# Performance work log

Hardware: AMD Instinct MI355X
Metric: run time of the kernel (lower is better)

## Reference

```python
import jax, jax.numpy as jnp
import numpy as np

N_NODES = 128
F = 64            # hidden channels (64x0e + 64x1o)
N_RBF = 8
H_R = 64          # radial MLP hidden
L = 2             # num_interactions
R_MAX = 5.0
AVG_NEIGH = 127.0
G_DIM = 16
N_SPECIES = 5

# static fully-connected edge list (no self edges): E = n*(n-1)
_idx = np.arange(N_NODES)
_s, _r = np.meshgrid(_idx, _idx, indexing='ij')
_mask = _s != _r
SENDERS = jnp.asarray(_s[_mask])    # [E]
RECEIVERS = jnp.asarray(_r[_mask])  # [E]


def setup_inputs() -> dict:
    key = jax.random.key(0)
    ks = jax.random.split(key, 12)
    inp = {
        'positions': jax.random.normal(ks[0], (32, N_NODES, 3), jnp.float32),
        'node_features': jax.random.randint(ks[1], (32, N_NODES), 0, N_SPECIES),
        'global_features': jax.random.normal(ks[2], (32, G_DIM), jnp.float32),
        # learned parameters
        'embed': jax.random.normal(ks[3], (N_SPECIES, F), jnp.float32) * 0.1,
        'glob_w': jax.random.normal(ks[4], (G_DIM, F), jnp.float32) * 0.1,
        'rbf_w1': jax.random.normal(ks[5], (L, N_RBF, H_R), jnp.float32) * 0.3,
        'rbf_b1': jnp.zeros((L, H_R), jnp.float32),
        'rbf_w2': jax.random.normal(ks[6], (L, H_R, 3 * F), jnp.float32) * 0.1,
        'ws': jax.random.normal(ks[7], (L, F, F), jnp.float32) * 0.1,
        'wv': jax.random.normal(ks[8], (L, F, F), jnp.float32) * 0.1,
        'wout': jax.random.normal(ks[9], (F,), jnp.float32) * 0.1,
        'final_scaling': jnp.ones((), jnp.float32),
    }
    return inp


def _rbf(d):
    # gaussian radial basis on [0, r_max]
    centers = jnp.linspace(0.0, R_MAX, N_RBF)
    width = R_MAX / N_RBF
    return jnp.exp(-((d[:, None] - centers) ** 2) / (2.0 * width * width))  # [E, N_RBF]


def _single(pos, species, glob, embed, glob_w, rbf_w1, rbf_b1, rbf_w2, ws, wv, wout, final_scaling):
    # graph construction + edge vectors
    edge_vec = pos[RECEIVERS] - pos[SENDERS]                 # [E,3]
    d = jnp.sqrt(jnp.sum(edge_vec ** 2, axis=-1) + 1e-12)   # [E]
    unit = edge_vec / d[:, None]                             # [E,3]
    phi = _rbf(d)                                            # [E,N_RBF]

    # node embedding (species one-hot lookup) conditioned on global features
    s = embed[species] + glob @ glob_w                       # [n,F] scalars
    v = jnp.zeros((N_NODES, F, 3), pos.dtype)                # [n,F,3] vectors

    for l in range(L):
        rw = jax.nn.silu(phi @ rbf_w1[l] + rbf_b1[l]) @ rbf_w2[l]  # [E,3F]
        r1, r2, r3 = jnp.split(rw, 3, axis=-1)               # each [E,F]
        ms = r1 * s[SENDERS]                                 # [E,F]
        mv = r2[..., None] * v[SENDERS] + (r3 * s[SENDERS])[..., None] * unit[:, None, :]  # [E,F,3]
        agg_s = jax.ops.segment_sum(ms, RECEIVERS, num_segments=N_NODES) / AVG_NEIGH
        agg_v = jax.ops.segment_sum(mv, RECEIVERS, num_segments=N_NODES) / AVG_NEIGH
        s = s + agg_s @ ws[l]
        v = v + jnp.einsum('nfd,fg->ngd', agg_v, wv[l])

    out = jnp.einsum('nfd,f->nd', v, wout)                   # equivariant readout [n,3]
    return (out - pos) * final_scaling


def reference(positions, node_features, global_features, embed, glob_w, rbf_w1,
              rbf_b1, rbf_w2, ws, wv, wout, final_scaling):
    fn = lambda p, sp, g: _single(p, sp, g, embed, glob_w, rbf_w1, rbf_b1,
                                  rbf_w2, ws, wv, wout, final_scaling)
    return jax.vmap(fn)(positions, node_features, global_features)
```

## Files before the change

kernel.cpp:

```cpp
#include <hip/hip_runtime.h>
#include <hip/hip_bf16.h>


#define NN 128
#define BB 32
#define FF 64

using f32x4  = __attribute__((ext_vector_type(4))) float;
using short8 = __attribute__((ext_vector_type(8))) short;
using half4  = __attribute__((ext_vector_type(4))) _Float16;

__device__ __forceinline__ unsigned short f2bf(float x) {
    unsigned int u = __float_as_uint(x);
    u += 0x7fff + ((u >> 16) & 1);
    return (unsigned short)(u >> 16);
}
__device__ __forceinline__ unsigned int f2bf_fast32(float x) {
    return (__float_as_uint(x) + 0x8000u) >> 16;
}

__global__ __launch_bounds__(256) void setup_kernel(
    const float* __restrict__ w2,
    const float* __restrict__ ws,
    const float* __restrict__ wv,
    const float* __restrict__ rbf_w1,
    const float* __restrict__ rbf_b1,
    const int* __restrict__ species, const float* __restrict__ glob,
    const float* __restrict__ embed, const float* __restrict__ glob_w,
    short* __restrict__ w2frag,
    float* __restrict__ wT4,
    _Float16* __restrict__ w1A,
    float* __restrict__ s)
{
    const int blk = blockIdx.x;
    if (blk < 192) {
        const int tid = blk * 256 + threadIdx.x;
        const int NFRAG = 24576;
        if (tid < NFRAG) {
            const int e  = tid & 7;
            const int l  = (tid >> 3) & 63;
            const int ks = (tid >> 9) & 1;
            const int q  = tid >> 10;
            const int nt = q % 3;
            const int wv_ = (q / 3) & 3;
            const int layer = q / 12;
            const int col = nt * 64 + wv_ * 16 + (l & 15);
            const int hb  = ks * 32 + (l >> 4) * 8 + e;
            const float val = w2[layer * 64 * 192 + hb * 192 + col] * (1.0f / 127.0f);
            w2frag[tid] = (short)f2bf(val);
        }
        const int tid2 = tid - NFRAG;
        if (tid2 >= 0 && tid2 < 16384) {
            const int c   = tid2 & 3;
            const int g   = (tid2 >> 2) & 63;
            const int ff4 = (tid2 >> 8) & 15;
            const int m   = (tid2 >> 12) & 1;
            const int layer = tid2 >> 13;
            const float* src = (m == 0 ? ws : wv) + layer * 4096;
            wT4[tid2] = src[(ff4 * 4 + c) * 64 + g];
        }
        const int tid3 = tid - NFRAG - 16384;
        if (tid3 >= 0 && tid3 < 2048) {
            const int e  = tid3 & 3;
            const int l  = (tid3 >> 2) & 63;
            const int wv_ = (tid3 >> 8) & 3;
            const int layer = tid3 >> 10;
            const int k = (l >> 4) * 4 + e;
            const int h = wv_ * 16 + (l & 15);
            float val = 0.0f;
            if (k < 8)       val = rbf_w1[layer * 512 + k * 64 + h];
            else if (k == 8) val = rbf_b1[layer * 64 + h];
            w1A[tid3] = (_Float16)val;
        }
    } else {
        const int node = (blk - 192) * 4 + (threadIdx.x >> 6);
        const int b = node >> 7;
        const int f = threadIdx.x & 63;
        const int sp = species[node];
        float acc = embed[sp * FF + f];
#pragma unroll
        for (int k = 0; k < 16; ++k)
            acc = fmaf(glob[b * 16 + k], glob_w[k * FF + f], acc);
        s[node * FF + f] = acc;
    }
}

template<int LAYER>
__global__ __launch_bounds__(256, 2) void msg_kernel(
    const float* __restrict__ pos,
    const float* __restrict__ s_in,
    const float* __restrict__ v_in,
    const half4* __restrict__ w1Abuf,
    const short* __restrict__ w2frag,
    const float* __restrict__ wT4,
    const float* __restrict__ wout,
    const float* __restrict__ scale,
    float* __restrict__ s_out,
    float* __restrict__ v_out,
    float* __restrict__ out)
{
    __shared__ unsigned short hid_lds[NN * 64];
    __shared__ float4 unit_lds[NN];
    __shared__ __align__(16) char phi_pool[NN * 32];
    float4 (*agg4)[16] = (float4(*)[16])phi_pool;

    const int blk = blockIdx.x;
    const int xcd = blk & 7;
    const int idx = blk >> 3;
    const int b = xcd * 4 + (idx >> 7);
    const int i = idx & 127;

    const int t = threadIdx.x;
    const int w = t >> 6;
    const int l = t & 63;
    const int node = b * NN + i;
    const float* pb = pos + b * NN * 3;

    const int f    = w * 16 + (l & 15);
    const int jsub = (l >> 4) * 4;
    const float* sb = s_in + b * NN * FF;
    const float4* vb4 = (LAYER > 0) ? ((const float4*)v_in) + b * NN * FF : nullptr;

    float sP[4]; float4 vP[4];
#pragma unroll
    for (int reg = 0; reg < 4; ++reg) {
        const int j = jsub + reg;
        sP[reg] = sb[j * FF + f];
        if (LAYER > 0) vP[reg] = vb4[j * FF + f];
    }

    short8 bfrag[3][2];
    {
        const short8* wf = (const short8*)w2frag;
#pragma unroll
        for (int nt = 0; nt < 3; ++nt) {
            if (LAYER == 0 && nt == 1) continue;
#pragma unroll
            for (int ks = 0; ks < 2; ++ks)
                bfrag[nt][ks] = wf[((w * 3 + nt) * 2 + ks) * 64 + l];
        }
    }

    {
        const int j = t & 127;
        const int half = t >> 7;
        const float dx = pb[i * 3 + 0] - pb[j * 3 + 0];
        const float dy = pb[i * 3 + 1] - pb[j * 3 + 1];
        const float dz = pb[i * 3 + 2] - pb[j * 3 + 2];
        const float d2 = fmaf(dx, dx, fmaf(dy, dy, fmaf(dz, dz, 1e-12f)));
        const float inv = __builtin_amdgcn_rsqf(d2);
        const float dd = d2 * inv;
        if (half == 0)
            unit_lds[j] = make_float4(dx * inv, dy * inv, dz * inv, 0.0f);
        const _Float16 zf = (_Float16)0.f;
        half4 ph;
#pragma unroll
        for (int r = 0; r < 4; ++r) {
            const float td = dd - (float)(half * 4 + r) * (5.0f / 7.0f);
            ph[r] = (_Float16)__expf(td * td * -1.28f);
        }
        if (j == i) ph = (half4){zf, zf, zf, zf};
        char* rowp = phi_pool + j * 32;
        const int swz = ((j >> 2) & 3) << 3;
        *(half4*)(rowp + ((half * 8) ^ swz)) = ph;
        if (half == 0) {
            half4 bias = {(j == i) ? zf : (_Float16)1.0f, zf, zf, zf};
            *(half4*)(rowp + (16 ^ swz)) = bias;
        } else {
            *(half4*)(rowp + (24 ^ swz)) = (half4){zf, zf, zf, zf};
        }
    }
    __syncthreads();

    {
        const half4 w1a = w1Abuf[w * 64 + l];
        const int jcol = l & 15;
        const int chunk = (l >> 4) * 8;
        const int hbyte = w * 32 + (l >> 4) * 8;
#pragma unroll
        for (int mt = 0; mt < 8; ++mt) {
            const int j = mt * 16 + jcol;
            const half4 bphi = *(const half4*)(
                phi_pool + j * 32 + (chunk ^ (((j >> 2) & 3) << 3)));
            f32x4 pre = __builtin_amdgcn_mfma_f32_16x16x16f16(
                w1a, bphi, (f32x4){0.f, 0.f, 0.f, 0.f}, 0, 0, 0);
            unsigned int pk[2];
#pragma unroll
            for (int p = 0; p < 2; ++p) {
                float sv[2];
#pragma unroll
                for (int q = 0; q < 2; ++q) {
                    const float z = pre[p * 2 + q];
                    const float ex = __expf(-z);
                    sv[q] = z * __builtin_amdgcn_rcpf(1.0f + ex);
                }
                pk[p] = f2bf_fast32(sv[0]) | (f2bf_fast32(sv[1]) << 16);
            }
            const int byte = j * 128 + (hbyte ^ ((j & 7) << 4));
            *(uint2*)((char*)hid_lds + byte) = make_uint2(pk[0], pk[1]);
        }
    }
    __syncthreads();

    float accs = 0.f, av0 = 0.f, av1 = 0.f, av2 = 0.f;

#pragma unroll
    for (int mt = 0; mt < 8; ++mt) {
        const int jA = mt * 16 + (l & 15);
        const int base = jA * 128;
        const int sw = (jA & 7) << 4;
        const short8 a0 = *(const short8*)((const char*)hid_lds + base + (((l >> 4) * 16 +  0) ^ sw));
        const short8 a1 = *(const short8*)((const char*)hid_lds + base + (((l >> 4) * 16 + 64) ^ sw));

        f32x4 c0 = (f32x4){0.f, 0.f, 0.f, 0.f};
        f32x4 c1 = (f32x4){0.f, 0.f, 0.f, 0.f};
        f32x4 c2 = (f32x4){0.f, 0.f, 0.f, 0.f};
        c0 = __builtin_amdgcn_mfma_f32_16x16x32_bf16(a0, bfrag[0][0], c0, 0, 0, 0);
        c0 = __builtin_amdgcn_mfma_f32_16x16x32_bf16(a1, bfrag[0][1], c0, 0, 0, 0);
        if (LAYER > 0) {
            c1 = __builtin_amdgcn_mfma_f32_16x16x32_bf16(a0, bfrag[1][0], c1, 0, 0, 0);
            c1 = __builtin_amdgcn_mfma_f32_16x16x32_bf16(a1, bfrag[1][1], c1, 0, 0, 0);
        }
        c2 = __builtin_amdgcn_mfma_f32_16x16x32_bf16(a0, bfrag[2][0], c2, 0, 0, 0);
        c2 = __builtin_amdgcn_mfma_f32_16x16x32_bf16(a1, bfrag[2][1], c2, 0, 0, 0);

        float sN[4]; float4 vN[4];
        if (mt < 7) {
#pragma unroll
            for (int reg = 0; reg < 4; ++reg) {
                const int j = (mt + 1) * 16 + jsub + reg;
                sN[reg] = sb[j * FF + f];
                if (LAYER > 0) vN[reg] = vb4[j * FF + f];
            }
        }

#pragma unroll
        for (int reg = 0; reg < 4; ++reg) {
            const int j  = mt * 16 + jsub + reg;
            const float r1 = c0[reg];
            const float r2 = c1[reg];
            const float r3 = c2[reg];
            const float sj = sP[reg];
            const float r3s = r3 * sj;
            const float4 u = unit_lds[j];
            accs = fmaf(r1, sj, accs);
            av0 = fmaf(r3s, u.x, av0);
            av1 = fmaf(r3s, u.y, av1);
            av2 = fmaf(r3s, u.z, av2);
            if (LAYER > 0) {
                av0 = fmaf(r2, vP[reg].x, av0);
                av1 = fmaf(r2, vP[reg].y, av1);
                av2 = fmaf(r2, vP[reg].z, av2);
            }
        }
#pragma unroll
        for (int reg = 0; reg < 4; ++reg) {
            sP[reg] = sN[reg];
            if (LAYER > 0) vP[reg] = vN[reg];
        }
    }

    accs += __shfl_xor(accs, 16, 64); accs += __shfl_xor(accs, 32, 64);
    av0  += __shfl_xor(av0, 16, 64);  av0  += __shfl_xor(av0, 32, 64);
    av1  += __shfl_xor(av1, 16, 64);  av1  += __shfl_xor(av1, 32, 64);
    av2  += __shfl_xor(av2, 16, 64);  av2  += __shfl_xor(av2, 32, 64);
    if (l < 16) {
        ((float*)agg4)[0 * 64 + f] = accs;
        ((float*)agg4)[1 * 64 + f] = av0;
        ((float*)agg4)[2 * 64 + f] = av1;
        ((float*)agg4)[3 * 64 + f] = av2;
    }
    __syncthreads();

    const int g = l;
    const float4* wv4 = (const float4*)wT4;
    if (LAYER == 0) {
        const int m = (w == 0) ? 0 : 1;
        const int row = (w == 0) ? 0 : w;
        float a = (w == 0) ? s_in[node * FF + g] : 0.0f;
#pragma unroll
        for (int k = 0; k < 16; ++k) {
            const float4 w4 = wv4[(m * 16 + k) * 64 + g];
            const float4 a4 = agg4[row][k];
            a = fmaf(a4.x, w4.x, a); a = fmaf(a4.y, w4.y, a);
            a = fmaf(a4.z, w4.z, a); a = fmaf(a4.w, w4.w, a);
        }
        if (w == 0) s_out[node * FF + g] = a;
        else        v_out[(node * FF + g) * 4 + (w - 1)] = a;
    } else {
        if (w > 0) {
            const int d = w - 1;
            float a = v_in[(node * FF + g) * 4 + d];
#pragma unroll
            for (int k = 0; k < 16; ++k) {
                const float4 w4 = wv4[(16 + k) * 64 + g];
                const float4 a4 = agg4[w][k];
                a = fmaf(a4.x, w4.x, a); a = fmaf(a4.y, w4.y, a);
                a = fmaf(a4.z, w4.z, a); a = fmaf(a4.w, w4.w, a);
            }
            float p = a * wout[g];
#pragma unroll
            for (int off = 1; off < 64; off <<= 1)
                p += __shfl_xor(p, off, 64);
            if (l == 0)
                out[node * 3 + d] = (p - pos[node * 3 + d]) * scale[0];
        }
    }
}

extern "C" void kernel_launch(void* const* d_in, const int* in_sizes, int n_in,
                              void* d_out, int out_size, void* d_ws, size_t ws_size,
                              hipStream_t stream) {
    const float* pos     = (const float*)d_in[0];
    const int*   species = (const int*)  d_in[1];
    const float* glob    = (const float*)d_in[2];
    const float* embed   = (const float*)d_in[3];
    const float* glob_w  = (const float*)d_in[4];
    const float* rbf_w1  = (const float*)d_in[5];
    const float* rbf_b1  = (const float*)d_in[6];
    const float* rbf_w2  = (const float*)d_in[7];
    const float* ws      = (const float*)d_in[8];
    const float* wv      = (const float*)d_in[9];
    const float* wout    = (const float*)d_in[10];
    const float* scale   = (const float*)d_in[11];

    float* wsf = (float*)d_ws;
    float* s0     = wsf;
    float* s1     = wsf + 262144;
    float* v1     = wsf + 524288;
    short* w2frag = (short*)(wsf + 1572864);
    float* wT4    = wsf + 1585152;
    _Float16* w1A = (_Float16*)(wsf + 1601536);
    float* outp = (float*)d_out;

    setup_kernel<<<dim3(192 + BB * NN / 4), 256, 0, stream>>>(
        rbf_w2, ws, wv, rbf_w1, rbf_b1, species, glob, embed, glob_w,
        w2frag, wT4, w1A, s0);

    msg_kernel<0><<<dim3(NN * BB), 256, 0, stream>>>(
        pos, s0, nullptr,
        (const half4*)w1A, w2frag, wT4, wout, scale,
        s1, v1, nullptr);

    msg_kernel<1><<<dim3(NN * BB), 256, 0, stream>>>(
        pos, s1, v1,
        (const half4*)(w1A + 1024), w2frag + 12288, wT4 + 8192, wout, scale,
        nullptr, nullptr, outp);
}
```

Before: 78.35 us.

## Process two receiver nodes per block to reuse sender features and weights

Each block now handles two receiver nodes instead of one, halving the grid. The per-sender s/v loads, weight fragments and wT4 reads are shared across both receivers, and two independent MFMA chains give more instruction-level parallelism. The cost is doubled LDS (about 41KB per block), more registers, and fewer blocks, which may lower occupancy and wave-level parallelism.

```diff
diff --git a/kernel.cpp b/kernel.cpp
--- a/kernel.cpp
+++ b/kernel.cpp
@@ -99,21 +99,19 @@
     float* __restrict__ v_out,
     float* __restrict__ out)
 {
-    __shared__ unsigned short hid_lds[NN * 64];
-    __shared__ float4 unit_lds[NN];
-    __shared__ __align__(16) char phi_pool[NN * 32];
-    float4 (*agg4)[16] = (float4(*)[16])phi_pool;
+    __shared__ unsigned short hid_lds[2 * NN * 64];
+    __shared__ float4 unit_lds[2][NN];
+    __shared__ __align__(16) char phi_pool[2 * NN * 32];
 
     const int blk = blockIdx.x;
     const int xcd = blk & 7;
     const int idx = blk >> 3;
-    const int b = xcd * 4 + (idx >> 7);
-    const int i = idx & 127;
+    const int b = xcd * 4 + (idx >> 6);
+    const int i0 = (idx & 63) * 2;
 
     const int t = threadIdx.x;
     const int w = t >> 6;
     const int l = t & 63;
-    const int node = b * NN + i;
     const float* pb = pos + b * NN * 3;
 
     const int f    = w * 16 + (l & 15);
@@ -143,32 +141,33 @@
 
     {
         const int j = t & 127;
-        const int half = t >> 7;
-        const float dx = pb[i * 3 + 0] - pb[j * 3 + 0];
-        const float dy = pb[i * 3 + 1] - pb[j * 3 + 1];
-        const float dz = pb[i * 3 + 2] - pb[j * 3 + 2];
+        const int rr = t >> 7;
+        const int ie = i0 + rr;
+        const float dx = pb[ie * 3 + 0] - pb[j * 3 + 0];
+        const float dy = pb[ie * 3 + 1] - pb[j * 3 + 1];
+        const float dz = pb[ie * 3 + 2] - pb[j * 3 + 2];
         const float d2 = fmaf(dx, dx, fmaf(dy, dy, fmaf(dz, dz, 1e-12f)));
         const float inv = __builtin_amdgcn_rsqf(d2);
         const float dd = d2 * inv;
-        if (half == 0)
-            unit_lds[j] = make_float4(dx * inv, dy * inv, dz * inv, 0.0f);
+        unit_lds[rr][j] = make_float4(dx * inv, dy * inv, dz * inv, 0.0f);
         const _Float16 zf = (_Float16)0.f;
-        half4 ph;
+        const half4 z4 = {zf, zf, zf, zf};
+        half4 ph0, ph1;
 #pragma unroll
         for (int r = 0; r < 4; ++r) {
-            const float td = dd - (float)(half * 4 + r) * (5.0f / 7.0f);
-            ph[r] = (_Float16)__expf(td * td * -1.28f);
-        }
-        if (j == i) ph = (half4){zf, zf, zf, zf};
-        char* rowp = phi_pool + j * 32;
+            const float td0 = dd - (float)r * (5.0f / 7.0f);
+            ph0[r] = (_Float16)__expf(td0 * td0 * -1.28f);
+            const float td1 = dd - (float)(4 + r) * (5.0f / 7.0f);
+            ph1[r] = (_Float16)__expf(td1 * td1 * -1.28f);
+        }
+        if (j == ie) { ph0 = z4; ph1 = z4; }
+        char* rowp = phi_pool + rr * 4096 + j * 32;
         const int swz = ((j >> 2) & 3) << 3;
-        *(half4*)(rowp + ((half * 8) ^ swz)) = ph;
-        if (half == 0) {
-            half4 bias = {(j == i) ? zf : (_Float16)1.0f, zf, zf, zf};
-            *(half4*)(rowp + (16 ^ swz)) = bias;
-        } else {
-            *(half4*)(rowp + (24 ^ swz)) = (half4){zf, zf, zf, zf};
-        }
+        *(half4*)(rowp + (0 ^ swz))  = ph0;
+        *(half4*)(rowp + (8 ^ swz))  = ph1;
+        half4 bias = {(j == ie) ? zf : (_Float16)1.0f, zf, zf, zf};
+        *(half4*)(rowp + (16 ^ swz)) = bias;
+        *(half4*)(rowp + (24 ^ swz)) = z4;
     }
     __syncthreads();
 
@@ -178,51 +177,62 @@
         const int chunk = (l >> 4) * 8;
         const int hbyte = w * 32 + (l >> 4) * 8;
 #pragma unroll
-        for (int mt = 0; mt < 8; ++mt) {
-            const int j = mt * 16 + jcol;
-            const half4 bphi = *(const half4*)(
-                phi_pool + j * 32 + (chunk ^ (((j >> 2) & 3) << 3)));
-            f32x4 pre = __builtin_amdgcn_mfma_f32_16x16x16f16(
-                w1a, bphi, (f32x4){0.f, 0.f, 0.f, 0.f}, 0, 0, 0);
-            unsigned int pk[2];
-#pragma unroll
-            for (int p = 0; p < 2; ++p) {
-                float sv[2];
-#pragma unroll
-                for (int q = 0; q < 2; ++q) {
-                    const float z = pre[p * 2 + q];
-                    const float ex = __expf(-z);
-                    sv[q] = z * __builtin_amdgcn_rcpf(1.0f + ex);
+        for (int rr = 0; rr < 2; ++rr) {
+            const char* phir = phi_pool + rr * 4096;
+            char* hidr = (char*)hid_lds + rr * 16384;
+#pragma unroll
+            for (int mt = 0; mt < 8; ++mt) {
+                const int j = mt * 16 + jcol;
+                const half4 bphi = *(const half4*)(
+                    phir + j * 32 + (chunk ^ (((j >> 2) & 3) << 3)));
+                f32x4 pre = __builtin_amdgcn_mfma_f32_16x16x16f16(
+                    w1a, bphi, (f32x4){0.f, 0.f, 0.f, 0.f}, 0, 0, 0);
+                unsigned int pk[2];
+#pragma unroll
+                for (int p = 0; p < 2; ++p) {
+                    float sv[2];
+#pragma unroll
+                    for (int q = 0; q < 2; ++q) {
+                        const float z = pre[p * 2 + q];
+                        const float ex = __expf(-z);
+                        sv[q] = z * __builtin_amdgcn_rcpf(1.0f + ex);
+                    }
+                    pk[p] = f2bf_fast32(sv[0]) | (f2bf_fast32(sv[1]) << 16);
                 }
-                pk[p] = f2bf_fast32(sv[0]) | (f2bf_fast32(sv[1]) << 16);
-            }
-            const int byte = j * 128 + (hbyte ^ ((j & 7) << 4));
-            *(uint2*)((char*)hid_lds + byte) = make_uint2(pk[0], pk[1]);
+                const int byte = j * 128 + (hbyte ^ ((j & 7) << 4));
+                *(uint2*)(hidr + byte) = make_uint2(pk[0], pk[1]);
+            }
         }
     }
     __syncthreads();
 
-    float accs = 0.f, av0 = 0.f, av1 = 0.f, av2 = 0.f;
+    float a0s = 0.f, a0x = 0.f, a0y = 0.f, a0z = 0.f;
+    float a1s = 0.f, a1x = 0.f, a1y = 0.f, a1z = 0.f;
 
 #pragma unroll
     for (int mt = 0; mt < 8; ++mt) {
         const int jA = mt * 16 + (l & 15);
         const int base = jA * 128;
         const int sw = (jA & 7) << 4;
-        const short8 a0 = *(const short8*)((const char*)hid_lds + base + (((l >> 4) * 16 +  0) ^ sw));
-        const short8 a1 = *(const short8*)((const char*)hid_lds + base + (((l >> 4) * 16 + 64) ^ sw));
+        const int o0 = base + (((l >> 4) * 16 +  0) ^ sw);
+        const int o1 = base + (((l >> 4) * 16 + 64) ^ sw);
+        const char* hp = (const char*)hid_lds;
+        const short8 a0r0 = *(const short8*)(hp + o0);
+        const short8 a1r0 = *(const short8*)(hp + o1);
+        const short8 a0r1 = *(const short8*)(hp + 16384 + o0);
+        const short8 a1r1 = *(const short8*)(hp + 16384 + o1);
 
         f32x4 c0 = (f32x4){0.f, 0.f, 0.f, 0.f};
         f32x4 c1 = (f32x4){0.f, 0.f, 0.f, 0.f};
         f32x4 c2 = (f32x4){0.f, 0.f, 0.f, 0.f};
-        c0 = __builtin_amdgcn_mfma_f32_16x16x32_bf16(a0, bfrag[0][0], c0, 0, 0, 0);
-        c0 = __builtin_amdgcn_mfma_f32_16x16x32_bf16(a1, bfrag[0][1], c0, 0, 0, 0);
+        c0 = __builtin_amdgcn_mfma_f32_16x16x32_bf16(a0r0, bfrag[0][0], c0, 0, 0, 0);
+        c0 = __builtin_amdgcn_mfma_f32_16x16x32_bf16(a1r0, bfrag[0][1], c0, 0, 0, 0);
         if (LAYER > 0) {
-            c1 = __builtin_amdgcn_mfma_f32_16x16x32_bf16(a0, bfrag[1][0], c1, 0, 0, 0);
-            c1 = __builtin_amdgcn_mfma_f32_16x16x32_bf16(a1, bfrag[1][1], c1, 0, 0, 0);
-        }
-        c2 = __builtin_amdgcn_mfma_f32_16x16x32_bf16(a0, bfrag[2][0], c2, 0, 0, 0);
-        c2 = __builtin_amdgcn_mfma_f32_16x16x32_bf16(a1, bfrag[2][1], c2, 0, 0, 0);
+            c1 = __builtin_amdgcn_mfma_f32_16x16x32_bf16(a0r0, bfrag[1][0], c1, 0, 0, 0);
+            c1 = __builtin_amdgcn_mfma_f32_16x16x32_bf16(a1r0, bfrag[1][1], c1, 0, 0, 0);
+        }
+        c2 = __builtin_amdgcn_mfma_f32_16x16x32_bf16(a0r0, bfrag[2][0], c2, 0, 0, 0);
+        c2 = __builtin_amdgcn_mfma_f32_16x16x32_bf16(a1r0, bfrag[2][1], c2, 0, 0, 0);
 
         float sN[4]; float4 vN[4];
         if (mt < 7) {
@@ -237,22 +247,49 @@
 #pragma unroll
         for (int reg = 0; reg < 4; ++reg) {
             const int j  = mt * 16 + jsub + reg;
-            const float r1 = c0[reg];
-            const float r2 = c1[reg];
-            const float r3 = c2[reg];
             const float sj = sP[reg];
-            const float r3s = r3 * sj;
-            const float4 u = unit_lds[j];
-            accs = fmaf(r1, sj, accs);
-            av0 = fmaf(r3s, u.x, av0);
-            av1 = fmaf(r3s, u.y, av1);
-            av2 = fmaf(r3s, u.z, av2);
+            const float r3s = c2[reg] * sj;
+            const float4 u = unit_lds[0][j];
+            a0s = fmaf(c0[reg], sj, a0s);
+            a0x = fmaf(r3s, u.x, a0x);
+            a0y = fmaf(r3s, u.y, a0y);
+            a0z = fmaf(r3s, u.z, a0z);
             if (LAYER > 0) {
-                av0 = fmaf(r2, vP[reg].x, av0);
-                av1 = fmaf(r2, vP[reg].y, av1);
-                av2 = fmaf(r2, vP[reg].z, av2);
-            }
-        }
+                a0x = fmaf(c1[reg], vP[reg].x, a0x);
+                a0y = fmaf(c1[reg], vP[reg].y, a0y);
+                a0z = fmaf(c1[reg], vP[reg].z, a0z);
+            }
+        }
+
+        c0 = (f32x4){0.f, 0.f, 0.f, 0.f};
+        c1 = (f32x4){0.f, 0.f, 0.f, 0.f};
+        c2 = (f32x4){0.f, 0.f, 0.f, 0.f};
+        c0 = __builtin_amdgcn_mfma_f32_16x16x32_bf16(a0r1, bfrag[0][0], c0, 0, 0, 0);
+        c0 = __builtin_amdgcn_mfma_f32_16x16x32_bf16(a1r1, bfrag[0][1], c0, 0, 0, 0);
+        if (LAYER > 0) {
+            c1 = __builtin_amdgcn_mfma_f32_16x16x32_bf16(a0r1, bfrag[1][0], c1, 0, 0, 0);
+            c1 = __builtin_amdgcn_mfma_f32_16x16x32_bf16(a1r1, bfrag[1][1], c1, 0, 0, 0);
+        }
+        c2 = __builtin_amdgcn_mfma_f32_16x16x32_bf16(a0r1, bfrag[2][0], c2, 0, 0, 0);
+        c2 = __builtin_amdgcn_mfma_f32_16x16x32_bf16(a1r1, bfrag[2][1], c2, 0, 0, 0);
+
+#pragma unroll
+        for (int reg = 0; reg < 4; ++reg) {
+            const int j  = mt * 16 + jsub + reg;
+            const float sj = sP[reg];
+            const float r3s = c2[reg] * sj;
+            const float4 u = unit_lds[1][j];
+            a1s = fmaf(c0[reg], sj, a1s);
+            a1x = fmaf(r3s, u.x, a1x);
+            a1y = fmaf(r3s, u.y, a1y);
+            a1z = fmaf(r3s, u.z, a1z);
+            if (LAYER > 0) {
+                a1x = fmaf(c1[reg], vP[reg].x, a1x);
+                a1y = fmaf(c1[reg], vP[reg].y, a1y);
+                a1z = fmaf(c1[reg], vP[reg].z, a1z);
+            }
+        }
+
 #pragma unroll
         for (int reg = 0; reg < 4; ++reg) {
             sP[reg] = sN[reg];
@@ -260,50 +297,82 @@
         }
     }
 
-    accs += __shfl_xor(accs, 16, 64); accs += __shfl_xor(accs, 32, 64);
-    av0  += __shfl_xor(av0, 16, 64);  av0  += __shfl_xor(av0, 32, 64);
-    av1  += __shfl_xor(av1, 16, 64);  av1  += __shfl_xor(av1, 32, 64);
-    av2  += __shfl_xor(av2, 16, 64);  av2  += __shfl_xor(av2, 32, 64);
+    a0s += __shfl_xor(a0s, 16, 64); a0s += __shfl_xor(a0s, 32, 64);
+    a0x += __shfl_xor(a0x, 16, 64); a0x += __shfl_xor(a0x, 32, 64);
+    a0y += __shfl_xor(a0y, 16, 64); a0y += __shfl_xor(a0y, 32, 64);
+    a0z += __shfl_xor(a0z, 16, 64); a0z += __shfl_xor(a0z, 32, 64);
+    a1s += __shfl_xor(a1s, 16, 64); a1s += __shfl_xor(a1s, 32, 64);
+    a1x += __shfl_xor(a1x, 16, 64); a1x += __shfl_xor(a1x, 32, 64);
+    a1y += __shfl_xor(a1y, 16, 64); a1y += __shfl_xor(a1y, 32, 64);
+    a1z += __shfl_xor(a1z, 16, 64); a1z += __shfl_xor(a1z, 32, 64);
     if (l < 16) {
-        ((float*)agg4)[0 * 64 + f] = accs;
-        ((float*)agg4)[1 * 64 + f] = av0;
-        ((float*)agg4)[2 * 64 + f] = av1;
-        ((float*)agg4)[3 * 64 + f] = av2;
+        float* aggf = (float*)phi_pool;
+        aggf[0 * 256 + 0 * 64 + f] = a0s;
+        aggf[0 * 256 + 1 * 64 + f] = a0x;
+        aggf[0 * 256 + 2 * 64 + f] = a0y;
+        aggf[0 * 256 + 3 * 64 + f] = a0z;
+        aggf[1 * 256 + 0 * 64 + f] = a1s;
+        aggf[1 * 256 + 1 * 64 + f] = a1x;
+        aggf[1 * 256 + 2 * 64 + f] = a1y;
+        aggf[1 * 256 + 3 * 64 + f] = a1z;
     }
     __syncthreads();
 
     const int g = l;
+    const int node0 = b * NN + i0;
+    const int node1 = node0 + 1;
     const float4* wv4 = (const float4*)wT4;
+    const float4* ag = (const float4*)phi_pool;
     if (LAYER == 0) {
         const int m = (w == 0) ? 0 : 1;
         const int row = (w == 0) ? 0 : w;
-        float a = (w == 0) ? s_in[node * FF + g] : 0.0f;
+        float a0 = (w == 0) ? s_in[node0 * FF + g] : 0.0f;
+        float a1 = (w == 0) ? s_in[node1 * FF + g] : 0.0f;
 #pragma unroll
         for (int k = 0; k < 16; ++k) {
             const float4 w4 = wv4[(m * 16 + k) * 64 + g];
-            const float4 a4 = agg4[row][k];
-            a = fmaf(a4.x, w4.x, a); a = fmaf(a4.y, w4.y, a);
-            a = fmaf(a4.z, w4.z, a); a = fmaf(a4.w, w4.w, a);
-        }
-        if (w == 0) s_out[node * FF + g] = a;
-        else        v_out[(node * FF + g) * 4 + (w - 1)] = a;
+            const float4 x0 = ag[0 * 64 + row * 16 + k];
+            const float4 x1 = ag[1 * 64 + row * 16 + k];
+            a0 = fmaf(x0.x, w4.x, a0); a0 = fmaf(x0.y, w4.y, a0);
+            a0 = fmaf(x0.z, w4.z, a0); a0 = fmaf(x0.w, w4.w, a0);
+            a1 = fmaf(x1.x, w4.x, a1); a1 = fmaf(x1.y, w4.y, a1);
+            a1 = fmaf(x1.z, w4.z, a1); a1 = fmaf(x1.w, w4.w, a1);
+        }
+        if (w == 0) {
+            s_out[node0 * FF + g] = a0;
+            s_out[node1 * FF + g] = a1;
+        } else {
+            v_out[(node0 * FF + g) * 4 + (w - 1)] = a0;
+            v_out[(node1 * FF + g) * 4 + (w - 1)] = a1;
+        }
     } else {
         if (w > 0) {
             const int d = w - 1;
-            float a = v_in[(node * FF + g) * 4 + d];
+            float a0 = v_in[(node0 * FF + g) * 4 + d];
+            float a1 = v_in[(node1 * FF + g) * 4 + d];
 #pragma unroll
             for (int k = 0; k < 16; ++k) {
                 const float4 w4 = wv4[(16 + k) * 64 + g];
-                const float4 a4 = agg4[w][k];
-                a = fmaf(a4.x, w4.x, a); a = fmaf(a4.y, w4.y, a);
-                a = fmaf(a4.z, w4.z, a); a = fmaf(a4.w, w4.w, a);
-            }
-            float p = a * wout[g];
-#pragma unroll
-            for (int off = 1; off < 64; off <<= 1)
-                p += __shfl_xor(p, off, 64);
-            if (l == 0)
-                out[node * 3 + d] = (p - pos[node * 3 + d]) * scale[0];
+                const float4 x0 = ag[0 * 64 + w * 16 + k];
+                const float4 x1 = ag[1 * 64 + w * 16 + k];
+                a0 = fmaf(x0.x, w4.x, a0); a0 = fmaf(x0.y, w4.y, a0);
+                a0 = fmaf(x0.z, w4.z, a0); a0 = fmaf(x0.w, w4.w, a0);
+                a1 = fmaf(x1.x, w4.x, a1); a1 = fmaf(x1.y, w4.y, a1);
+                a1 = fmaf(x1.z, w4.z, a1); a1 = fmaf(x1.w, w4.w, a1);
+            }
+            const float wg = wout[g];
+            float p0 = a0 * wg;
+            float p1 = a1 * wg;
+#pragma unroll
+            for (int off = 1; off < 64; off <<= 1) {
+                p0 += __shfl_xor(p0, off, 64);
+                p1 += __shfl_xor(p1, off, 64);
+            }
+            if (l == 0) {
+                const float sc = scale[0];
+                out[node0 * 3 + d] = (p0 - pos[node0 * 3 + d]) * sc;
+                out[node1 * 3 + d] = (p1 - pos[node1 * 3 + d]) * sc;
+            }
         }
     }
 }
@@ -337,12 +406,12 @@
         rbf_w2, ws, wv, rbf_w1, rbf_b1, species, glob, embed, glob_w,
         w2frag, wT4, w1A, s0);
 
-    msg_kernel<0><<<dim3(NN * BB), 256, 0, stream>>>(
+    msg_kernel<0><<<dim3(NN * BB / 2), 256, 0, stream>>>(
         pos, s0, nullptr,
         (const half4*)w1A, w2frag, wT4, wout, scale,
         s1, v1, nullptr);
 
-    msg_kernel<1><<<dim3(NN * BB), 256, 0, stream>>>(
+    msg_kernel<1><<<dim3(NN * BB / 2), 256, 0, stream>>>(
         pos, s1, v1,
         (const half4*)(w1A + 1024), w2frag + 12288, wT4 + 8192, wout, scale,
         nullptr, nullptr, outp);
```

New measurement: 67.72 us (median of 2 runs). -13.6%, faster.
